# Optimization experiments

Hardware: AMD Instinct MI355X
Metric: run time of the kernel (lower is better)

The kernel has to match this reference:

```python
import jax, jax.numpy as jnp
import numpy as np

D_MODEL = 1024
NUM_HEADS = 16
HEAD_DIM = D_MODEL // NUM_HEADS
B, S = 4, 2048


def setup_inputs() -> dict:
    key = jax.random.key(0)
    ks = jax.random.split(key, 6)
    scale = 1.0 / np.sqrt(D_MODEL)
    return {
        "q": jax.random.normal(ks[0], (B, S, D_MODEL), dtype=jnp.float32),
        "k": jax.random.normal(ks[1], (B, S, D_MODEL), dtype=jnp.float32),
        "v": jax.random.normal(ks[2], (B, S, D_MODEL), dtype=jnp.float32),
        "Wq": jax.random.normal(ks[3], (D_MODEL, D_MODEL), dtype=jnp.float32) * scale,
        "Wk": jax.random.normal(ks[4], (D_MODEL, D_MODEL), dtype=jnp.float32) * scale,
        "Wv": jax.random.normal(ks[5], (D_MODEL, D_MODEL), dtype=jnp.float32) * scale,
    }


def reference(q, k, v, Wq, Wk, Wv):
    b, s, d = q.shape
    # nn.Linear(bias=False): x @ W.T
    qp = jnp.einsum('bsd,ed->bse', q, Wq)
    kp = jnp.einsum('bsd,ed->bse', k, Wk)
    vp = jnp.einsum('bsd,ed->bse', v, Wv)
    # split heads -> (B, H, S, Dh)
    qh = qp.reshape(b, s, NUM_HEADS, HEAD_DIM).transpose(0, 2, 1, 3)
    kh = kp.reshape(b, s, NUM_HEADS, HEAD_DIM).transpose(0, 2, 1, 3)
    vh = vp.reshape(b, s, NUM_HEADS, HEAD_DIM).transpose(0, 2, 1, 3)
    scores = jnp.einsum('bhqd,bhkd->bhqk', qh, kh) / jnp.sqrt(jnp.float32(HEAD_DIM))
    attn = jax.nn.softmax(scores, axis=-1)
    att = jnp.einsum('bhqk,bhkd->bhqd', attn, vh)
    # NOTE: faithful to the source, which does a raw .view (no head transpose back)
    return att.reshape(b, s, d)
```

## Files before the change

### kernel.cpp

```cpp
#include <hip/hip_runtime.h>
#include <hip/hip_bf16.h>
#include <stdint.h>

#define D_MODEL 1024
#define NHEAD   16
#define HDIM    64
#define BATCH   4
#define SEQ     2048
#define NTOK    (BATCH*SEQ)

typedef __bf16          b16x8 __attribute__((ext_vector_type(8)));
typedef unsigned short  u16x8 __attribute__((ext_vector_type(8)));
typedef unsigned short  u16x4 __attribute__((ext_vector_type(4)));
typedef float           f32x4 __attribute__((ext_vector_type(4)));

__device__ __forceinline__ unsigned short f2b(float f) {
  union { float f; uint32_t u; } c; c.f = f;
  return (unsigned short)((c.u + 0x7FFFu + ((c.u >> 16) & 1u)) >> 16);
}

__device__ __forceinline__ uint32_t cvtpk(float lo, float hi) {
  uint32_t r;
  asm("v_cvt_pk_bf16_f32 %0, %1, %2" : "=v"(r) : "v"(lo), "v"(hi));
  return r;
}

__device__ __forceinline__ u16x4 pk4(f32x4 x) {
  union { uint32_t u[2]; u16x4 v; } r;
  r.u[0] = cvtpk(x[0], x[1]);
  r.u[1] = cvtpk(x[2], x[3]);
  return r.v;
}

__device__ __forceinline__ u16x8 pk8(f32x4 a, f32x4 b) {
  union { uint32_t u[4]; u16x8 v; } r;
  r.u[0] = cvtpk(a[0], a[1]);
  r.u[1] = cvtpk(a[2], a[3]);
  r.u[2] = cvtpk(b[0], b[1]);
  r.u[3] = cvtpk(b[2], b[3]);
  return r.v;
}

__global__ __launch_bounds__(256, 4)
void proj_gemm_kernel(const float* __restrict__ q, const float* __restrict__ k,
                      const float* __restrict__ v, const float* __restrict__ Wq,
                      const float* __restrict__ Wk, const float* __restrict__ Wv,
                      unsigned short* __restrict__ qp, unsigned short* __restrict__ kp,
                      unsigned short* __restrict__ vt) {
  __shared__ unsigned short As[2][128 * 32];
  __shared__ unsigned short Bs[2][128 * 32];

  int bid = blockIdx.x;
  int swz = (bid & 7) * 192 + (bid >> 3);
  int which = swz >> 9;
  int rr = swz & 511;
  int tm = rr >> 3, tn = rr & 7;

  const float* X = (which == 0) ? q : ((which == 1) ? k : v);
  const float* W = (which == 0) ? Wq : ((which == 1) ? Wk : Wv);

  int tid  = threadIdx.x;
  int lane = tid & 63;
  int w    = tid >> 6;
  int g    = lane >> 4;
  int c    = lane & 15;
  int wr   = (w >> 1) * 64;
  int wc   = (w & 1) * 64;

  f32x4 acc[4][4];
#pragma unroll
  for (int m = 0; m < 4; m++)
#pragma unroll
    for (int n = 0; n < 4; n++) acc[m][n] = (f32x4){0.f, 0.f, 0.f, 0.f};

  int srow = tid >> 2;
  int sseg = tid & 3;
  const float* Ag = X + (size_t)(tm * 128 + srow) * D_MODEL + sseg * 8;
  const float* Bg = W + (size_t)(tn * 128 + srow) * D_MODEL + sseg * 8;

  int wbyte = srow * 64 + ((sseg ^ ((srow >> 1) & 3)) << 4);
  int rco   = ((g ^ ((c >> 1) & 3)) << 4);
  int raoff = (wr + c) * 64 + rco;
  int rboff = (wc + c) * 64 + rco;

  f32x4 ra[2][2], rb[2][2];
#pragma unroll
  for (int r = 0; r < 2; r++)
#pragma unroll
    for (int h = 0; h < 2; h++) {
      ra[r][h] = *(const f32x4*)(Ag + (size_t)r * 64 * D_MODEL + h * 4);
      rb[r][h] = *(const f32x4*)(Bg + (size_t)r * 64 * D_MODEL + h * 4);
    }
  *(u16x8*)((char*)As[0] + wbyte)        = pk8(ra[0][0], ra[0][1]);
  *(u16x8*)((char*)As[0] + wbyte + 4096) = pk8(ra[1][0], ra[1][1]);
  *(u16x8*)((char*)Bs[0] + wbyte)        = pk8(rb[0][0], rb[0][1]);
  *(u16x8*)((char*)Bs[0] + wbyte + 4096) = pk8(rb[1][0], rb[1][1]);

  for (int kt = 0; kt < 32; kt++) {
    __syncthreads();
    if (kt < 31) {
#pragma unroll
      for (int r = 0; r < 2; r++)
#pragma unroll
        for (int h = 0; h < 2; h++) {
          ra[r][h] = *(const f32x4*)(Ag + (size_t)r * 64 * D_MODEL + (kt + 1) * 32 + h * 4);
          rb[r][h] = *(const f32x4*)(Bg + (size_t)r * 64 * D_MODEL + (kt + 1) * 32 + h * 4);
        }
    }
    const char* Ab = (const char*)As[kt & 1];
    const char* Bb = (const char*)Bs[kt & 1];
    u16x8 af[4], bf[4];
#pragma unroll
    for (int m = 0; m < 4; m++)
      af[m] = *(const u16x8*)(Ab + raoff + m * 1024);
#pragma unroll
    for (int n = 0; n < 4; n++)
      bf[n] = *(const u16x8*)(Bb + rboff + n * 1024);
#pragma unroll
    for (int m = 0; m < 4; m++)
#pragma unroll
      for (int n = 0; n < 4; n++)
        acc[m][n] = __builtin_amdgcn_mfma_f32_16x16x32_bf16(
            __builtin_bit_cast(b16x8, af[m]), __builtin_bit_cast(b16x8, bf[n]),
            acc[m][n], 0, 0, 0);
    if (kt < 31) {
      char* An = (char*)As[(kt + 1) & 1];
      char* Bn = (char*)Bs[(kt + 1) & 1];
      *(u16x8*)(An + wbyte)        = pk8(ra[0][0], ra[0][1]);
      *(u16x8*)(An + wbyte + 4096) = pk8(ra[1][0], ra[1][1]);
      *(u16x8*)(Bn + wbyte)        = pk8(rb[0][0], rb[0][1]);
      *(u16x8*)(Bn + wbyte + 4096) = pk8(rb[1][0], rb[1][1]);
    }
  }

  int cbase = tn * 128 + wc;
  int rbase = tm * 128 + wr;
  if (which < 2) {
    unsigned short* OutP = (which == 0) ? qp : kp;
    float scale = (which == 0) ? 0.18033688f : 1.0f;
#pragma unroll
    for (int m = 0; m < 4; m++)
#pragma unroll
      for (int n = 0; n < 4; n++) {
        int e = cbase + n * 16 + c;
        int h = e >> 6, dh = e & 63;
#pragma unroll
        for (int j = 0; j < 4; j++) {
          int i = rbase + m * 16 + g * 4 + j;
          int b = i >> 11, s = i & 2047;
          OutP[(((size_t)(b * NHEAD + h)) * SEQ + s) * HDIM + dh] =
              f2b(acc[m][n][j] * scale);
        }
      }
  } else {
#pragma unroll
    for (int m = 0; m < 4; m++)
#pragma unroll
      for (int n = 0; n < 4; n++) {
        int e = cbase + n * 16 + c;
        int h = e >> 6, dh = e & 63;
        int i0 = rbase + m * 16 + g * 4;
        int b = i0 >> 11, s0 = i0 & 2047;
        *(u16x4*)&vt[(((size_t)(b * NHEAD + h)) * HDIM + dh) * SEQ + s0] = pk4(acc[m][n]);
      }
  }
}

#define KVB 64
__global__ __launch_bounds__(256, 3)
void attn_kernel(const unsigned short* __restrict__ qp,
                 const unsigned short* __restrict__ kp,
                 const unsigned short* __restrict__ vt,
                 float* __restrict__ out) {
  __shared__ __align__(16) char lds[2][16384];

  int bid = blockIdx.x;
  int swz = (bid & 7) * 128 + (bid >> 3);
  int bh = swz >> 4;
  int qb = swz & 15;

  int tid  = threadIdx.x;
  int lane = tid & 63;
  int w    = tid >> 6;
  int g    = lane >> 4;
  int c    = lane & 15;
  int chi  = c & 7;

  const unsigned short* Kg = kp + (size_t)bh * SEQ * HDIM;
  const unsigned short* Vg = vt + (size_t)bh * HDIM * SEQ;

  int q0 = qb * 128 + w * 32;
  u16x8 qf[2][2];
#pragma unroll
  for (int qg = 0; qg < 2; qg++)
#pragma unroll
    for (int h = 0; h < 2; h++)
      qf[qg][h] = *(const u16x8*)&qp[((size_t)bh * SEQ + q0 + qg * 16 + c) * HDIM + h * 32 + g * 8];

  f32x4 o[4][2];
#pragma unroll
  for (int d = 0; d < 4; d++)
#pragma unroll
    for (int qg = 0; qg < 2; qg++) o[d][qg] = (f32x4){0.f, 0.f, 0.f, 0.f};
  float l[2] = {0.f, 0.f};

  int koffA = c * 128 + ((g * 16) ^ (chi << 4));
  int koffB = c * 128 + (((64 + g * 16)) ^ (chi << 4));
  int voff[2][2];
#pragma unroll
  for (int w2 = 0; w2 < 2; w2++) {
    int b0 = w2 * 64 + g * 8;
    voff[w2][0] = 8192 + c * 128 + ((((b0      >> 4) ^ chi) << 4) + (b0 & 15));
    voff[w2][1] = 8192 + c * 128 + (((((b0+32) >> 4) ^ chi) << 4) + (b0 & 15));
  }
  int arow = tid >> 3, aseg = tid & 7;
  int kwo = arow * 128 + ((aseg * 16) ^ ((arow & 7) << 4));
  int vwo = 8192 + kwo;

  char* cur = lds[0];
  char* nxt = lds[1];

  u16x8 kreg[2], vreg[2];
  kreg[0] = *(const u16x8*)&Kg[(size_t)arow * HDIM + aseg * 8];
  kreg[1] = *(const u16x8*)&Kg[(size_t)(arow + 32) * HDIM + aseg * 8];
  vreg[0] = *(const u16x8*)&Vg[(size_t)arow * SEQ + aseg * 8];
  vreg[1] = *(const u16x8*)&Vg[(size_t)(arow + 32) * SEQ + aseg * 8];
  *(u16x8*)(cur + kwo)        = kreg[0];
  *(u16x8*)(cur + kwo + 4096) = kreg[1];
  *(u16x8*)(cur + vwo)        = vreg[0];
  *(u16x8*)(cur + vwo + 4096) = vreg[1];
  __syncthreads();

  for (int t = 0; t < SEQ / KVB; t++) {
    if (t < SEQ / KVB - 1) {
      int kv1 = (t + 1) * KVB;
      kreg[0] = *(const u16x8*)&Kg[(size_t)(kv1 + arow) * HDIM + aseg * 8];
      kreg[1] = *(const u16x8*)&Kg[(size_t)(kv1 + arow + 32) * HDIM + aseg * 8];
      vreg[0] = *(const u16x8*)&Vg[(size_t)arow * SEQ + kv1 + aseg * 8];
      vreg[1] = *(const u16x8*)&Vg[(size_t)(arow + 32) * SEQ + kv1 + aseg * 8];
    }

    f32x4 sf[4][2];
#pragma unroll
    for (int st = 0; st < 4; st++) {
      u16x8 kf0 = *(const u16x8*)(cur + koffA + st * 2048);
      u16x8 kf1 = *(const u16x8*)(cur + koffB + st * 2048);
#pragma unroll
      for (int qg = 0; qg < 2; qg++) {
        sf[st][qg] = __builtin_amdgcn_mfma_f32_16x16x32_bf16(
            __builtin_bit_cast(b16x8, kf0), __builtin_bit_cast(b16x8, qf[qg][0]),
            (f32x4){0.f, 0.f, 0.f, 0.f}, 0, 0, 0);
        sf[st][qg] = __builtin_amdgcn_mfma_f32_16x16x32_bf16(
            __builtin_bit_cast(b16x8, kf1), __builtin_bit_cast(b16x8, qf[qg][1]),
            sf[st][qg], 0, 0, 0);
      }
    }

    union { uint32_t u[4]; u16x8 v; } pb[2][2];
#pragma unroll
    for (int qg = 0; qg < 2; qg++) {
      float p[4][4];
#pragma unroll
      for (int st = 0; st < 4; st++)
#pragma unroll
        for (int j = 0; j < 4; j++) p[st][j] = exp2f(sf[st][qg][j]);
      float s01 = ((p[0][0] + p[0][1]) + (p[0][2] + p[0][3])) +
                  ((p[1][0] + p[1][1]) + (p[1][2] + p[1][3]));
      float s23 = ((p[2][0] + p[2][1]) + (p[2][2] + p[2][3])) +
                  ((p[3][0] + p[3][1]) + (p[3][2] + p[3][3]));
      l[qg] += s01 + s23;
#pragma unroll
      for (int w2 = 0; w2 < 2; w2++) {
        pb[w2][qg].u[0] = cvtpk(p[2*w2][0],   p[2*w2][1]);
        pb[w2][qg].u[1] = cvtpk(p[2*w2][2],   p[2*w2][3]);
        pb[w2][qg].u[2] = cvtpk(p[2*w2+1][0], p[2*w2+1][1]);
        pb[w2][qg].u[3] = cvtpk(p[2*w2+1][2], p[2*w2+1][3]);
      }
    }

#pragma unroll
    for (int w2 = 0; w2 < 2; w2++)
#pragma unroll
      for (int d = 0; d < 4; d++) {
        union { u16x4 h[2]; u16x8 v; } afu;
        afu.h[0] = *(const u16x4*)(cur + voff[w2][0] + d * 2048);
        afu.h[1] = *(const u16x4*)(cur + voff[w2][1] + d * 2048);
#pragma unroll
        for (int qg = 0; qg < 2; qg++)
          o[d][qg] = __builtin_amdgcn_mfma_f32_16x16x32_bf16(
              __builtin_bit_cast(b16x8, afu.v), __builtin_bit_cast(b16x8, pb[w2][qg].v),
              o[d][qg], 0, 0, 0);
      }

    if (t < SEQ / KVB - 1) {
      *(u16x8*)(nxt + kwo)        = kreg[0];
      *(u16x8*)(nxt + kwo + 4096) = kreg[1];
      *(u16x8*)(nxt + vwo)        = vreg[0];
      *(u16x8*)(nxt + vwo + 4096) = vreg[1];
    }
    __syncthreads();
    char* tmp = cur; cur = nxt; nxt = tmp;
  }

#pragma unroll
  for (int qg = 0; qg < 2; qg++) {
    l[qg] += __shfl_xor(l[qg], 16);
    l[qg] += __shfl_xor(l[qg], 32);
  }
#pragma unroll
  for (int qg = 0; qg < 2; qg++) {
    float inv = 1.f / l[qg];
    float* orow = out + ((size_t)bh * SEQ + q0 + qg * 16 + c) * HDIM;
#pragma unroll
    for (int d = 0; d < 4; d++) {
      f32x4 val;
#pragma unroll
      for (int j = 0; j < 4; j++) val[j] = o[d][qg][j] * inv;
      *(f32x4*)(orow + d * 16 + g * 4) = val;
    }
  }
}

extern "C" void kernel_launch(void* const* d_in, const int* in_sizes, int n_in,
                              void* d_out, int out_size, void* d_ws, size_t ws_size,
                              hipStream_t stream) {
  const float* q  = (const float*)d_in[0];
  const float* k  = (const float*)d_in[1];
  const float* v  = (const float*)d_in[2];
  const float* Wq = (const float*)d_in[3];
  const float* Wk = (const float*)d_in[4];
  const float* Wv = (const float*)d_in[5];

  unsigned short* qp = (unsigned short*)d_ws;
  unsigned short* kp = qp + (size_t)NTOK * D_MODEL;
  unsigned short* vt = kp + (size_t)NTOK * D_MODEL;
  float* out = (float*)d_out;

  hipLaunchKernelGGL(proj_gemm_kernel, dim3(1536), dim3(256), 0, stream,
                     q, k, v, Wq, Wk, Wv, qp, kp, vt);
  hipLaunchKernelGGL(attn_kernel, dim3(1024), dim3(256), 0, stream,
                     qp, kp, vt, out);
}
```

Measured before the change: 186.7 us.

## Pre-convert weights to bf16 and widen projection GEMM tile to 128x256

Adds a small kernel that converts the three fp32 weight matrices to bf16 in the workspace once per call, so the projection GEMM loads half the bytes for B and skips the B-side convert. The projection GEMM now uses 512-thread blocks with a 128x256 output tile, which halves the grid and reuses each A tile across twice as many columns, cutting redundant fp32 activation loads. The cost is an extra launch plus a 6 MB write/read of the bf16 weights, and larger blocks use more LDS per block, which may lower occupancy.

```diff
diff --git a/kernel.cpp b/kernel.cpp
--- a/kernel.cpp
+++ b/kernel.cpp
@@ -41,31 +41,40 @@
   return r.v;
 }
 
-__global__ __launch_bounds__(256, 4)
+__global__ __launch_bounds__(256, 8)
+void wconv_kernel(const float* __restrict__ Wq, const float* __restrict__ Wk,
+                  const float* __restrict__ Wv, unsigned short* __restrict__ wb) {
+  int bid = blockIdx.x;
+  const float* src = (bid < 512) ? Wq : ((bid < 1024) ? Wk : Wv);
+  int off = (bid & 511) * 2048 + threadIdx.x * 8;
+  f32x4 a = *(const f32x4*)(src + off);
+  f32x4 b = *(const f32x4*)(src + off + 4);
+  *(u16x8*)&wb[(size_t)(bid >> 9) * (D_MODEL * D_MODEL) + off] = pk8(a, b);
+}
+
+__global__ __launch_bounds__(512, 4)
 void proj_gemm_kernel(const float* __restrict__ q, const float* __restrict__ k,
-                      const float* __restrict__ v, const float* __restrict__ Wq,
-                      const float* __restrict__ Wk, const float* __restrict__ Wv,
+                      const float* __restrict__ v, const unsigned short* __restrict__ wb,
                       unsigned short* __restrict__ qp, unsigned short* __restrict__ kp,
                       unsigned short* __restrict__ vt) {
-  __shared__ unsigned short As[2][128 * 32];
-  __shared__ unsigned short Bs[2][128 * 32];
+  __shared__ __align__(16) char lds[2][24576];
 
   int bid = blockIdx.x;
-  int swz = (bid & 7) * 192 + (bid >> 3);
-  int which = swz >> 9;
-  int rr = swz & 511;
-  int tm = rr >> 3, tn = rr & 7;
+  int swz = (bid & 7) * 96 + (bid >> 3);
+  int which = swz >> 8;
+  int rr = swz & 255;
+  int tm = rr >> 2, tn = rr & 3;
 
   const float* X = (which == 0) ? q : ((which == 1) ? k : v);
-  const float* W = (which == 0) ? Wq : ((which == 1) ? Wk : Wv);
+  const unsigned short* W = wb + (size_t)which * (D_MODEL * D_MODEL);
 
   int tid  = threadIdx.x;
   int lane = tid & 63;
   int w    = tid >> 6;
   int g    = lane >> 4;
   int c    = lane & 15;
-  int wr   = (w >> 1) * 64;
-  int wc   = (w & 1) * 64;
+  int wr   = (w >> 2) * 64;
+  int wc   = (w & 3) * 64;
 
   f32x4 acc[4][4];
 #pragma unroll
@@ -73,49 +82,47 @@
 #pragma unroll
     for (int n = 0; n < 4; n++) acc[m][n] = (f32x4){0.f, 0.f, 0.f, 0.f};
 
-  int srow = tid >> 2;
-  int sseg = tid & 3;
-  const float* Ag = X + (size_t)(tm * 128 + srow) * D_MODEL + sseg * 8;
-  const float* Bg = W + (size_t)(tn * 128 + srow) * D_MODEL + sseg * 8;
-
-  int wbyte = srow * 64 + ((sseg ^ ((srow >> 1) & 3)) << 4);
+  int srowA = tid >> 2, ssegA = tid & 3;
+  int srowB = tid >> 1, ch0 = (tid & 1) * 2;
+  const float*          Ag = X + (size_t)(tm * 128 + srowA) * D_MODEL + ssegA * 8;
+  const unsigned short* Bg = W + (size_t)(tn * 256 + srowB) * D_MODEL + ch0 * 8;
+
+  int sA = (srowA >> 1) & 3;
+  int wbyteA = srowA * 64 + ((ssegA ^ sA) << 4);
+  int sB = (srowB >> 1) & 3;
+  int wbyteB0 = 8192 + srowB * 64 + ((ch0 ^ sB) << 4);
+  int wbyteB1 = 8192 + srowB * 64 + (((ch0 + 1) ^ sB) << 4);
+
   int rco   = ((g ^ ((c >> 1) & 3)) << 4);
   int raoff = (wr + c) * 64 + rco;
-  int rboff = (wc + c) * 64 + rco;
-
-  f32x4 ra[2][2], rb[2][2];
-#pragma unroll
-  for (int r = 0; r < 2; r++)
-#pragma unroll
-    for (int h = 0; h < 2; h++) {
-      ra[r][h] = *(const f32x4*)(Ag + (size_t)r * 64 * D_MODEL + h * 4);
-      rb[r][h] = *(const f32x4*)(Bg + (size_t)r * 64 * D_MODEL + h * 4);
-    }
-  *(u16x8*)((char*)As[0] + wbyte)        = pk8(ra[0][0], ra[0][1]);
-  *(u16x8*)((char*)As[0] + wbyte + 4096) = pk8(ra[1][0], ra[1][1]);
-  *(u16x8*)((char*)Bs[0] + wbyte)        = pk8(rb[0][0], rb[0][1]);
-  *(u16x8*)((char*)Bs[0] + wbyte + 4096) = pk8(rb[1][0], rb[1][1]);
+  int rboff = 8192 + (wc + c) * 64 + rco;
+
+  f32x4 ra0, ra1;
+  u16x8 rb0, rb1;
+  ra0 = *(const f32x4*)(Ag);
+  ra1 = *(const f32x4*)(Ag + 4);
+  rb0 = *(const u16x8*)(Bg);
+  rb1 = *(const u16x8*)(Bg + 8);
+  *(u16x8*)(lds[0] + wbyteA)  = pk8(ra0, ra1);
+  *(u16x8*)(lds[0] + wbyteB0) = rb0;
+  *(u16x8*)(lds[0] + wbyteB1) = rb1;
 
   for (int kt = 0; kt < 32; kt++) {
     __syncthreads();
     if (kt < 31) {
-#pragma unroll
-      for (int r = 0; r < 2; r++)
-#pragma unroll
-        for (int h = 0; h < 2; h++) {
-          ra[r][h] = *(const f32x4*)(Ag + (size_t)r * 64 * D_MODEL + (kt + 1) * 32 + h * 4);
-          rb[r][h] = *(const f32x4*)(Bg + (size_t)r * 64 * D_MODEL + (kt + 1) * 32 + h * 4);
-        }
-    }
-    const char* Ab = (const char*)As[kt & 1];
-    const char* Bb = (const char*)Bs[kt & 1];
+      ra0 = *(const f32x4*)(Ag + (kt + 1) * 32);
+      ra1 = *(const f32x4*)(Ag + (kt + 1) * 32 + 4);
+      rb0 = *(const u16x8*)(Bg + (kt + 1) * 32);
+      rb1 = *(const u16x8*)(Bg + (kt + 1) * 32 + 8);
+    }
+    const char* buf = lds[kt & 1];
     u16x8 af[4], bf[4];
 #pragma unroll
     for (int m = 0; m < 4; m++)
-      af[m] = *(const u16x8*)(Ab + raoff + m * 1024);
+      af[m] = *(const u16x8*)(buf + raoff + m * 1024);
 #pragma unroll
     for (int n = 0; n < 4; n++)
-      bf[n] = *(const u16x8*)(Bb + rboff + n * 1024);
+      bf[n] = *(const u16x8*)(buf + rboff + n * 1024);
 #pragma unroll
     for (int m = 0; m < 4; m++)
 #pragma unroll
@@ -124,16 +131,14 @@
             __builtin_bit_cast(b16x8, af[m]), __builtin_bit_cast(b16x8, bf[n]),
             acc[m][n], 0, 0, 0);
     if (kt < 31) {
-      char* An = (char*)As[(kt + 1) & 1];
-      char* Bn = (char*)Bs[(kt + 1) & 1];
-      *(u16x8*)(An + wbyte)        = pk8(ra[0][0], ra[0][1]);
-      *(u16x8*)(An + wbyte + 4096) = pk8(ra[1][0], ra[1][1]);
-      *(u16x8*)(Bn + wbyte)        = pk8(rb[0][0], rb[0][1]);
-      *(u16x8*)(Bn + wbyte + 4096) = pk8(rb[1][0], rb[1][1]);
-    }
-  }
-
-  int cbase = tn * 128 + wc;
+      char* nb = lds[(kt + 1) & 1];
+      *(u16x8*)(nb + wbyteA)  = pk8(ra0, ra1);
+      *(u16x8*)(nb + wbyteB0) = rb0;
+      *(u16x8*)(nb + wbyteB1) = rb1;
+    }
+  }
+
+  int cbase = tn * 256 + wc;
   int rbase = tm * 128 + wr;
   if (which < 2) {
     unsigned short* OutP = (which == 0) ? qp : kp;
@@ -334,10 +339,13 @@
   unsigned short* qp = (unsigned short*)d_ws;
   unsigned short* kp = qp + (size_t)NTOK * D_MODEL;
   unsigned short* vt = kp + (size_t)NTOK * D_MODEL;
+  unsigned short* wb = vt + (size_t)NTOK * D_MODEL;
   float* out = (float*)d_out;
 
-  hipLaunchKernelGGL(proj_gemm_kernel, dim3(1536), dim3(256), 0, stream,
-                     q, k, v, Wq, Wk, Wv, qp, kp, vt);
+  hipLaunchKernelGGL(wconv_kernel, dim3(1536), dim3(256), 0, stream,
+                     Wq, Wk, Wv, wb);
+  hipLaunchKernelGGL(proj_gemm_kernel, dim3(768), dim3(512), 0, stream,
+                     q, k, v, wb, qp, kp, vt);
   hipLaunchKernelGGL(attn_kernel, dim3(1024), dim3(256), 0, stream,
                      qp, kp, vt, out);
 }
```

Result: slower. 191.7 us (+2.7%).

## Prepack weights to swizzled bf16 tiles and stream them via global_load_lds

Applied to the files above, without the earlier changes.

Adds a pre-pass kernel that converts Wq/Wk/Wv to bf16 and lays them out as pre-swizzled 8KB tiles, one per (matrix, column tile, k step). The projection GEMM then loads its B operand straight into LDS with global_load_lds instead of loading fp32 into registers, converting and storing. This is meant to halve weight read traffic in the GEMM and drop register staging and pack instructions, which also allows occupancy to rise from 4 to 5 blocks per CU. The cost is an extra kernel launch and an extra write and read of the packed weights each call.

```diff
diff --git a/kernel.cpp b/kernel.cpp
--- a/kernel.cpp
+++ b/kernel.cpp
@@ -41,14 +41,40 @@
   return r.v;
 }
 
-__global__ __launch_bounds__(256, 4)
+__device__ __forceinline__ void glds16(const void* g, void* l) {
+  __builtin_amdgcn_global_load_lds(
+      (const __attribute__((address_space(1))) unsigned int*)g,
+      (__attribute__((address_space(3))) unsigned int*)l, 16, 0, 0);
+}
+
+__global__ __launch_bounds__(256, 8)
+void wpack_kernel(const float* __restrict__ Wq, const float* __restrict__ Wk,
+                  const float* __restrict__ Wv, unsigned short* __restrict__ wsp) {
+  int bid = blockIdx.x;
+  int which = bid >> 8;
+  int tn = (bid >> 5) & 7;
+  int kt = bid & 31;
+  const float* W = (which == 0) ? Wq : ((which == 1) ? Wk : Wv);
+  int t = threadIdx.x;
+  int r = t >> 1;
+  int sw0 = (t & 1) * 2;
+  char* dst = (char*)wsp + (size_t)bid * 8192 + t * 32;
+  const float* src = W + (size_t)(tn * 128 + r) * D_MODEL + kt * 32;
+#pragma unroll
+  for (int i = 0; i < 2; i++) {
+    int s = (sw0 + i) ^ ((r >> 1) & 3);
+    f32x4 a = *(const f32x4*)(src + s * 8);
+    f32x4 b = *(const f32x4*)(src + s * 8 + 4);
+    *(u16x8*)(dst + i * 16) = pk8(a, b);
+  }
+}
+
+__global__ __launch_bounds__(256, 5)
 void proj_gemm_kernel(const float* __restrict__ q, const float* __restrict__ k,
-                      const float* __restrict__ v, const float* __restrict__ Wq,
-                      const float* __restrict__ Wk, const float* __restrict__ Wv,
+                      const float* __restrict__ v, const unsigned short* __restrict__ wsp,
                       unsigned short* __restrict__ qp, unsigned short* __restrict__ kp,
                       unsigned short* __restrict__ vt) {
-  __shared__ unsigned short As[2][128 * 32];
-  __shared__ unsigned short Bs[2][128 * 32];
+  __shared__ __align__(16) char lds[2][16384];
 
   int bid = blockIdx.x;
   int swz = (bid & 7) * 192 + (bid >> 3);
@@ -57,7 +83,7 @@
   int tm = rr >> 3, tn = rr & 7;
 
   const float* X = (which == 0) ? q : ((which == 1) ? k : v);
-  const float* W = (which == 0) ? Wq : ((which == 1) ? Wk : Wv);
+  const char* Bsrc = (const char*)wsp + (size_t)((which * 8 + tn) * 32) * 8192;
 
   int tid  = threadIdx.x;
   int lane = tid & 63;
@@ -73,49 +99,44 @@
 #pragma unroll
     for (int n = 0; n < 4; n++) acc[m][n] = (f32x4){0.f, 0.f, 0.f, 0.f};
 
-  int srow = tid >> 2;
-  int sseg = tid & 3;
+  int srow = tid >> 2, sseg = tid & 3;
   const float* Ag = X + (size_t)(tm * 128 + srow) * D_MODEL + sseg * 8;
-  const float* Bg = W + (size_t)(tn * 128 + srow) * D_MODEL + sseg * 8;
-
-  int wbyte = srow * 64 + ((sseg ^ ((srow >> 1) & 3)) << 4);
+  int wbyteA = srow * 64 + ((sseg ^ ((srow >> 1) & 3)) << 4);
+
   int rco   = ((g ^ ((c >> 1) & 3)) << 4);
   int raoff = (wr + c) * 64 + rco;
-  int rboff = (wc + c) * 64 + rco;
-
-  f32x4 ra[2][2], rb[2][2];
-#pragma unroll
-  for (int r = 0; r < 2; r++)
-#pragma unroll
-    for (int h = 0; h < 2; h++) {
-      ra[r][h] = *(const f32x4*)(Ag + (size_t)r * 64 * D_MODEL + h * 4);
-      rb[r][h] = *(const f32x4*)(Bg + (size_t)r * 64 * D_MODEL + h * 4);
-    }
-  *(u16x8*)((char*)As[0] + wbyte)        = pk8(ra[0][0], ra[0][1]);
-  *(u16x8*)((char*)As[0] + wbyte + 4096) = pk8(ra[1][0], ra[1][1]);
-  *(u16x8*)((char*)Bs[0] + wbyte)        = pk8(rb[0][0], rb[0][1]);
-  *(u16x8*)((char*)Bs[0] + wbyte + 4096) = pk8(rb[1][0], rb[1][1]);
+  int rboff = 8192 + (wc + c) * 64 + rco;
+
+  int bglane = w * 2048 + lane * 16;
+
+  f32x4 ra0 = *(const f32x4*)(Ag);
+  f32x4 ra1 = *(const f32x4*)(Ag + 4);
+  f32x4 ra2 = *(const f32x4*)(Ag + 64 * D_MODEL);
+  f32x4 ra3 = *(const f32x4*)(Ag + 64 * D_MODEL + 4);
+  glds16(Bsrc + bglane,        lds[0] + 8192 + w * 2048);
+  glds16(Bsrc + bglane + 1024, lds[0] + 8192 + w * 2048 + 1024);
+  *(u16x8*)(lds[0] + wbyteA)        = pk8(ra0, ra1);
+  *(u16x8*)(lds[0] + wbyteA + 4096) = pk8(ra2, ra3);
 
   for (int kt = 0; kt < 32; kt++) {
     __syncthreads();
+    char* nb = lds[(kt + 1) & 1];
     if (kt < 31) {
-#pragma unroll
-      for (int r = 0; r < 2; r++)
-#pragma unroll
-        for (int h = 0; h < 2; h++) {
-          ra[r][h] = *(const f32x4*)(Ag + (size_t)r * 64 * D_MODEL + (kt + 1) * 32 + h * 4);
-          rb[r][h] = *(const f32x4*)(Bg + (size_t)r * 64 * D_MODEL + (kt + 1) * 32 + h * 4);
-        }
-    }
-    const char* Ab = (const char*)As[kt & 1];
-    const char* Bb = (const char*)Bs[kt & 1];
+      ra0 = *(const f32x4*)(Ag + (kt + 1) * 32);
+      ra1 = *(const f32x4*)(Ag + (kt + 1) * 32 + 4);
+      ra2 = *(const f32x4*)(Ag + 64 * D_MODEL + (kt + 1) * 32);
+      ra3 = *(const f32x4*)(Ag + 64 * D_MODEL + (kt + 1) * 32 + 4);
+      glds16(Bsrc + (size_t)(kt + 1) * 8192 + bglane,        nb + 8192 + w * 2048);
+      glds16(Bsrc + (size_t)(kt + 1) * 8192 + bglane + 1024, nb + 8192 + w * 2048 + 1024);
+    }
+    const char* buf = lds[kt & 1];
     u16x8 af[4], bf[4];
 #pragma unroll
     for (int m = 0; m < 4; m++)
-      af[m] = *(const u16x8*)(Ab + raoff + m * 1024);
+      af[m] = *(const u16x8*)(buf + raoff + m * 1024);
 #pragma unroll
     for (int n = 0; n < 4; n++)
-      bf[n] = *(const u16x8*)(Bb + rboff + n * 1024);
+      bf[n] = *(const u16x8*)(buf + rboff + n * 1024);
 #pragma unroll
     for (int m = 0; m < 4; m++)
 #pragma unroll
@@ -124,12 +145,8 @@
             __builtin_bit_cast(b16x8, af[m]), __builtin_bit_cast(b16x8, bf[n]),
             acc[m][n], 0, 0, 0);
     if (kt < 31) {
-      char* An = (char*)As[(kt + 1) & 1];
-      char* Bn = (char*)Bs[(kt + 1) & 1];
-      *(u16x8*)(An + wbyte)        = pk8(ra[0][0], ra[0][1]);
-      *(u16x8*)(An + wbyte + 4096) = pk8(ra[1][0], ra[1][1]);
-      *(u16x8*)(Bn + wbyte)        = pk8(rb[0][0], rb[0][1]);
-      *(u16x8*)(Bn + wbyte + 4096) = pk8(rb[1][0], rb[1][1]);
+      *(u16x8*)(nb + wbyteA)        = pk8(ra0, ra1);
+      *(u16x8*)(nb + wbyteA + 4096) = pk8(ra2, ra3);
     }
   }
 
@@ -331,13 +348,16 @@
   const float* Wk = (const float*)d_in[4];
   const float* Wv = (const float*)d_in[5];
 
-  unsigned short* qp = (unsigned short*)d_ws;
-  unsigned short* kp = qp + (size_t)NTOK * D_MODEL;
-  unsigned short* vt = kp + (size_t)NTOK * D_MODEL;
+  unsigned short* qp  = (unsigned short*)d_ws;
+  unsigned short* kp  = qp + (size_t)NTOK * D_MODEL;
+  unsigned short* vt  = kp + (size_t)NTOK * D_MODEL;
+  unsigned short* wsp = vt + (size_t)NTOK * D_MODEL;
   float* out = (float*)d_out;
 
+  hipLaunchKernelGGL(wpack_kernel, dim3(768), dim3(256), 0, stream,
+                     Wq, Wk, Wv, wsp);
   hipLaunchKernelGGL(proj_gemm_kernel, dim3(1536), dim3(256), 0, stream,
-                     q, k, v, Wq, Wk, Wv, qp, kp, vt);
+                     q, k, v, wsp, qp, kp, vt);
   hipLaunchKernelGGL(attn_kernel, dim3(1024), dim3(256), 0, stream,
                      qp, kp, vt, out);
 }
```

New measurement: 200.4 us. 1.07x slower.
